# Optimization experiments

Measured on AMD Instinct MI355X. Metric: run time of the kernel, lower is better.

The kernel has to match this reference:

```python
import jax, jax.numpy as jnp
import numpy as np

N_NODES = 50000
N_EDGES = 800000
D_IN = 128
D_OUT = 128
NEG_SLOPE = 0.2


def setup_inputs() -> dict:
    key = jax.random.key(0)
    ks = jax.random.split(key, 6)
    stdv = 1.0 / np.sqrt(D_OUT)
    X = jax.random.normal(ks[0], (N_NODES, D_IN), dtype=jnp.float32)
    W = jax.random.uniform(ks[1], (D_IN, D_OUT), dtype=jnp.float32, minval=-stdv, maxval=stdv)
    W_r = jax.random.uniform(ks[2], (D_IN, D_OUT), dtype=jnp.float32, minval=-stdv, maxval=stdv)
    W_l = jax.random.uniform(ks[3], (D_IN, D_OUT), dtype=jnp.float32, minval=-stdv, maxval=stdv)
    src = jax.random.randint(ks[4], (N_EDGES,), 0, N_NODES, dtype=jnp.int32)
    dst = jax.random.randint(ks[5], (N_EDGES,), 0, N_NODES, dtype=jnp.int32)
    return {"X": X, "W": W, "W_r": W_r, "W_l": W_l, "src": src, "dst": dst}


def reference(X, W, W_r, W_l, src, dst):
    # Dense transforms (comb/agg feature paths)
    comb = X @ W            # [N, D_out]
    h_r = X @ W_r           # [N, D_out]
    h_l = X @ W_l           # [N, D_out]
    # SDDMM: per-edge score e_ij = dot(h_l[i], h_r[j]) at nonzeros of A
    e = jnp.sum(h_l[src] * h_r[dst], axis=-1)          # [E]
    e = jax.nn.leaky_relu(e, negative_slope=NEG_SLOPE)  # LeakyReLU(0.2) on edge values
    # SpMM aggregation: agg[i] = sum_{j in N(i)} e_ij * comb[j]
    msgs = e[:, None] * comb[dst]                       # [E, D_out]
    agg = jax.ops.segment_sum(msgs, src, num_segments=N_NODES)  # [N, D_out]
    return agg
```

## Files before the change

kernel.cpp:

```cpp
#include <hip/hip_runtime.h>
#include <hip/hip_bf16.h>

#define N_NODES 50000
#define N_EDGES 800000
#define D 128
#define NEG_SLOPE 0.2f
#define APAD 136

#define FB 196
#define BCAP 8192
#define CHUNK 2048
#define BIN_NBLK ((N_EDGES + CHUNK - 1) / CHUNK)
#define GROWS 64
#define GGRID ((N_NODES + GROWS - 1) / GROWS)
#define GEMM_LDS (D * APAD * 2 + GROWS * APAD * 2)

typedef __attribute__((ext_vector_type(8))) short bf16x8;
typedef __attribute__((ext_vector_type(4))) float f32x4;

__device__ inline unsigned short f2bf(float f) {
    union { float f; unsigned u; } v; v.f = f;
    const unsigned r = v.u + 0x7FFF + ((v.u >> 16) & 1);
    return (unsigned short)(r >> 16);
}
__device__ inline unsigned fbits(float f) { union { float f; unsigned u; } v; v.f = f; return v.u; }
__device__ inline float ffrom(unsigned u) { union { unsigned u; float f; } v; v.u = u; return v.f; }

__device__ inline void unpack8(const float4 raw, float* o) {
    const unsigned w0 = fbits(raw.x), w1 = fbits(raw.y), w2 = fbits(raw.z), w3 = fbits(raw.w);
    o[0] = ffrom(w0 << 16); o[1] = ffrom(w0 & 0xffff0000u);
    o[2] = ffrom(w1 << 16); o[3] = ffrom(w1 & 0xffff0000u);
    o[4] = ffrom(w2 << 16); o[5] = ffrom(w2 & 0xffff0000u);
    o[6] = ffrom(w3 << 16); o[7] = ffrom(w3 & 0xffff0000u);
}

__device__ inline int scan256_incl(int* arr, int t, int v) {
    arr[t] = v; __syncthreads();
#pragma unroll
    for (int off = 1; off < 256; off <<= 1) {
        const int u = (t >= off) ? arr[t - off] : 0;
        __syncthreads();
        arr[t] += u;
        __syncthreads();
    }
    return arr[t];
}

__device__ __forceinline__ void stage_B_lds(unsigned short* Bs, const ushort* __restrict__ BT) {
    const int tid = threadIdx.x;
#pragma unroll
    for (int i = 0; i < 8; ++i) {
        const int idx = tid + i * 256;
        const int row = idx >> 4;
        const int c8 = (idx & 15) << 3;
        const float4 v = ((const float4*)BT)[idx];
        *(float4*)&Bs[row * APAD + c8] = v;
    }
}

template <bool OUT_F32>
__device__ __forceinline__ void mfma_from_lds(const unsigned short* Bs,
                                              const unsigned short* As,
                                              int rb, float* __restrict__ Cf,
                                              ushort* __restrict__ Cb, int nrows) {
    const int tid = threadIdx.x;
    const int w = tid >> 6, lane = tid & 63, m = lane & 15, kq = lane >> 4;
    f32x4 acc[8] = {};
    const unsigned short* Arow = &As[(w * 16 + m) * APAD + kq * 8];
#pragma unroll
    for (int kc = 0; kc < 4; ++kc) {
        const bf16x8 af = *(const bf16x8*)(Arow + kc * 32);
#pragma unroll
        for (int t2 = 0; t2 < 8; ++t2) {
            const bf16x8 bf = *(const bf16x8*)&Bs[(t2 * 16 + m) * APAD + kc * 32 + kq * 8];
            acc[t2] = __builtin_amdgcn_mfma_f32_16x16x32_bf16(af, bf, acc[t2], 0, 0, 0);
        }
    }
    const int orow0 = rb + w * 16 + kq * 4;
#pragma unroll
    for (int t2 = 0; t2 < 8; ++t2) {
#pragma unroll
        for (int r = 0; r < 4; ++r) {
            const int row = orow0 + r;
            if (row < nrows) {
                const size_t o = (size_t)row * D + t2 * 16 + m;
                if (OUT_F32) Cf[o] = acc[t2][r];
                else         Cb[o] = f2bf(acc[t2][r]);
            }
        }
    }
}

__global__ __launch_bounds__(256) void prep_kernel(const float* __restrict__ W_l,
                                                   const float* __restrict__ W_r,
                                                   const float* __restrict__ W,
                                                   ushort* __restrict__ MbT,
                                                   ushort* __restrict__ WbT,
                                                   int* __restrict__ bucket_fill) {
    if (blockIdx.x == 0) bucket_fill[threadIdx.x] = 0;
    const int a = blockIdx.x * 2 + (threadIdx.x >> 7);
    const int b2 = threadIdx.x & 127;
    float acc = 0.f;
#pragma unroll
    for (int c = 0; c < D; c += 4) {
        const float4 wl = *(const float4*)(W_l + a * D + c);
        const float4 wr = *(const float4*)(W_r + b2 * D + c);
        acc += wl.x * wr.x + wl.y * wr.y + wl.z * wr.z + wl.w * wr.w;
    }
    MbT[b2 * D + a] = f2bf(acc);
    WbT[b2 * D + a] = f2bf(W[a * D + b2]);
}

__global__ __launch_bounds__(256) void k1_kernel(const int* __restrict__ src,
                                                 const int* __restrict__ dst,
                                                 int* __restrict__ bucket_fill,
                                                 int2* __restrict__ binned,
                                                 const ushort* __restrict__ MbT,
                                                 const float4* __restrict__ Xf4,
                                                 ushort* __restrict__ Xb,
                                                 ushort* __restrict__ hMb) {
    __shared__ __align__(16) char smem[GEMM_LDS];
    const int bx = blockIdx.x;
    const int t = threadIdx.x;

    if (bx < BIN_NBLK) {
        int*  hist     = (int*)smem;
        int*  bstart   = hist + 256;
        int*  reserveS = bstart + 256;
        int*  fillL    = reserveS + 256;
        int2* pairs    = (int2*)(fillL + 256);
        int*  targ     = (int*)(pairs + CHUNK);
        const int e0 = bx * CHUNK;

        hist[t] = 0;
        __syncthreads();

        int s[8], d[8], b[8];
#pragma unroll
        for (int i = 0; i < 8; ++i) {
            const int e = e0 + i * 256 + t;
            if (e < N_EDGES) {
                s[i] = src[e]; d[i] = dst[e]; b[i] = s[i] >> 8;
                atomicAdd(&hist[b[i]], 1);
            } else b[i] = -1;
        }
        __syncthreads();
        const int hv = hist[t];
        const int incl = scan256_incl(bstart, t, hv);
        const int mystart = incl - hv;
        reserveS[t] = hv ? atomicAdd(&bucket_fill[t], hv) : 0;
        __syncthreads();
        bstart[t] = mystart;
        fillL[t] = mystart;
        __syncthreads();
#pragma unroll
        for (int i = 0; i < 8; ++i) {
            if (b[i] >= 0) {
                const int p = atomicAdd(&fillL[b[i]], 1);
                pairs[p] = make_int2(s[i], d[i]);
                const int pos = reserveS[b[i]] + (p - bstart[b[i]]);
                targ[p] = (pos < BCAP) ? (b[i] * BCAP + pos) : -1;
            }
        }
        __syncthreads();
        const int nval = min(CHUNK, N_EDGES - e0);
        for (int j = t; j < nval; j += 256)
            if (targ[j] >= 0) binned[targ[j]] = pairs[j];
    } else {
        unsigned short* Bs = (unsigned short*)smem;
        unsigned short* As = Bs + D * APAD;
        const int rb = (bx - BIN_NBLK) * GROWS;

        stage_B_lds(Bs, MbT);
#pragma unroll
        for (int i = 0; i < 4; ++i) {
            const int f2 = t + i * 256;
            const int row = f2 >> 4;
            const int c8 = (f2 & 15) << 3;
            ushort4 lo = {0, 0, 0, 0}, hi = {0, 0, 0, 0};
            if (rb + row < N_NODES) {
                const float4 a = Xf4[(size_t)(rb + row) * 32 + (c8 >> 2)];
                const float4 b = Xf4[(size_t)(rb + row) * 32 + (c8 >> 2) + 1];
                lo.x = f2bf(a.x); lo.y = f2bf(a.y); lo.z = f2bf(a.z); lo.w = f2bf(a.w);
                hi.x = f2bf(b.x); hi.y = f2bf(b.y); hi.z = f2bf(b.z); hi.w = f2bf(b.w);
                ushort* gp = Xb + (size_t)(rb + row) * D + c8;
                *(ushort4*)gp = lo;
                *(ushort4*)(gp + 4) = hi;
            }
            *(ushort4*)&As[row * APAD + c8] = lo;
            *(ushort4*)&As[row * APAD + c8 + 4] = hi;
        }
        __syncthreads();
        mfma_from_lds<false>(Bs, As, rb, nullptr, hMb, N_NODES);
    }
}

__global__ __launch_bounds__(512) void fine_kernel(const int2* __restrict__ binned,
                                                   const int* __restrict__ bucket_fill,
                                                   int* __restrict__ offsets,
                                                   int* __restrict__ sorted_dst) {
    __shared__ int cntS[256];
    __shared__ int nh[256];
    __shared__ int ex[256];
    __shared__ int fill[256];
    __shared__ int dstbuf[BCAP];
    const int b = blockIdx.x;
    const int t = threadIdx.x;

    if (t < 256) cntS[t] = (t < FB) ? bucket_fill[t] : 0;
    __syncthreads();
#pragma unroll
    for (int off = 1; off < 256; off <<= 1) {
        const int u = (t >= off && t < 256) ? cntS[t - off] : 0;
        __syncthreads();
        if (t < 256) cntS[t] += u;
        __syncthreads();
    }
    const int base = (b == 0) ? 0 : cntS[b - 1];
    int cnt = cntS[b] - base;
    if (cnt > BCAP) cnt = BCAP;

    if (t < 256) nh[t] = 0;
    __syncthreads();
    const int2* bb = binned + (size_t)b * BCAP;
    for (int e = t; e < cnt; e += 512) atomicAdd(&nh[bb[e].x & 255], 1);
    __syncthreads();
    const int v = (t < 256) ? nh[t] : 0;
    if (t < 256) ex[t] = v;
    __syncthreads();
#pragma unroll
    for (int off = 1; off < 256; off <<= 1) {
        const int u = (t >= off && t < 256) ? ex[t - off] : 0;
        __syncthreads();
        if (t < 256) ex[t] += u;
        __syncthreads();
    }
    if (t < 256) {
        const int mystart = ex[t] - v;
        const int node = b * 256 + t;
        if (node < N_NODES) offsets[node] = base + mystart;
        fill[t] = mystart;
    }
    __syncthreads();
    for (int e = t; e < cnt; e += 512) {
        const int2 sd = bb[e];
        const int p = atomicAdd(&fill[sd.x & 255], 1);
        dstbuf[p] = sd.y;
    }
    __syncthreads();
    for (int j = t; j < cnt; j += 512)
        sorted_dst[base + j] = dstbuf[j];
}

__global__ __launch_bounds__(256) void spmm_kernel(const ushort* __restrict__ hMb,
                                                   const ushort* __restrict__ Xb,
                                                   const int* __restrict__ offsets,
                                                   const int* __restrict__ sorted_dst,
                                                   ushort* __restrict__ aggXb) {
    const int wave = threadIdx.x >> 6;
    const int lane = threadIdx.x & 63;
    const int node = blockIdx.x * 4 + wave;
    const int q = lane >> 4;
    const int ql = lane & 15;

    float hm[8];
    unpack8(*(const float4*)(hMb + (size_t)node * D + ql * 8), hm);

    const int start = offsets[node];
    const int end = (node == N_NODES - 1) ? N_EDGES : offsets[node + 1];

    float acc[8] = {0.f, 0.f, 0.f, 0.f, 0.f, 0.f, 0.f, 0.f};

    int idx = start + q;
    while (idx + 12 < end) {
        const int d0 = sorted_dst[idx];
        const int d1 = sorted_dst[idx + 4];
        const int d2 = sorted_dst[idx + 8];
        const int d3 = sorted_dst[idx + 12];
        const float4 r0 = *(const float4*)(Xb + (size_t)d0 * D + ql * 8);
        const float4 r1 = *(const float4*)(Xb + (size_t)d1 * D + ql * 8);
        const float4 r2 = *(const float4*)(Xb + (size_t)d2 * D + ql * 8);
        const float4 r3 = *(const float4*)(Xb + (size_t)d3 * D + ql * 8);
        float t0 = 0.f, t1 = 0.f, t2 = 0.f, t3 = 0.f;
        {
            float x[8];
            unpack8(r0, x);
#pragma unroll
            for (int j = 0; j < 8; ++j) t0 = fmaf(hm[j], x[j], t0);
            unpack8(r1, x);
#pragma unroll
            for (int j = 0; j < 8; ++j) t1 = fmaf(hm[j], x[j], t1);
            unpack8(r2, x);
#pragma unroll
            for (int j = 0; j < 8; ++j) t2 = fmaf(hm[j], x[j], t2);
            unpack8(r3, x);
#pragma unroll
            for (int j = 0; j < 8; ++j) t3 = fmaf(hm[j], x[j], t3);
        }
#pragma unroll
        for (int mm = 1; mm < 16; mm <<= 1) {
            t0 += __shfl_xor(t0, mm);
            t1 += __shfl_xor(t1, mm);
            t2 += __shfl_xor(t2, mm);
            t3 += __shfl_xor(t3, mm);
        }
        const float e0 = t0 > 0.f ? t0 : NEG_SLOPE * t0;
        const float e1 = t1 > 0.f ? t1 : NEG_SLOPE * t1;
        const float e2 = t2 > 0.f ? t2 : NEG_SLOPE * t2;
        const float e3 = t3 > 0.f ? t3 : NEG_SLOPE * t3;
        {
            float x[8];
            unpack8(r0, x);
#pragma unroll
            for (int j = 0; j < 8; ++j) acc[j] = fmaf(e0, x[j], acc[j]);
            unpack8(r1, x);
#pragma unroll
            for (int j = 0; j < 8; ++j) acc[j] = fmaf(e1, x[j], acc[j]);
            unpack8(r2, x);
#pragma unroll
            for (int j = 0; j < 8; ++j) acc[j] = fmaf(e2, x[j], acc[j]);
            unpack8(r3, x);
#pragma unroll
            for (int j = 0; j < 8; ++j) acc[j] = fmaf(e3, x[j], acc[j]);
        }
        idx += 16;
    }
    while (idx < end) {
        const int d0 = sorted_dst[idx];
        const float4 r0 = *(const float4*)(Xb + (size_t)d0 * D + ql * 8);
        float x[8];
        unpack8(r0, x);
        float t0 = 0.f;
#pragma unroll
        for (int j = 0; j < 8; ++j) t0 = fmaf(hm[j], x[j], t0);
#pragma unroll
        for (int mm = 1; mm < 16; mm <<= 1) t0 += __shfl_xor(t0, mm);
        const float e0 = t0 > 0.f ? t0 : NEG_SLOPE * t0;
#pragma unroll
        for (int j = 0; j < 8; ++j) acc[j] = fmaf(e0, x[j], acc[j]);
        idx += 4;
    }

#pragma unroll
    for (int j = 0; j < 8; ++j) {
        acc[j] += __shfl_xor(acc[j], 16);
        acc[j] += __shfl_xor(acc[j], 32);
    }
    if (q == 0) {
        ushort4 o0, o1;
        o0.x = f2bf(acc[0]); o0.y = f2bf(acc[1]); o0.z = f2bf(acc[2]); o0.w = f2bf(acc[3]);
        o1.x = f2bf(acc[4]); o1.y = f2bf(acc[5]); o1.z = f2bf(acc[6]); o1.w = f2bf(acc[7]);
        ushort* outp = aggXb + (size_t)node * D + ql * 8;
        *(ushort4*)outp = o0;
        *(ushort4*)(outp + 4) = o1;
    }
}

__global__ __launch_bounds__(256) void gemm2_kernel(const ushort* __restrict__ A,
                                                    const ushort* __restrict__ BT,
                                                    float* __restrict__ Cf) {
    __shared__ __align__(16) char smem[GEMM_LDS];
    unsigned short* Bs = (unsigned short*)smem;
    unsigned short* As = Bs + D * APAD;
    const int tid = threadIdx.x;
    const int rb = blockIdx.x * GROWS;

    stage_B_lds(Bs, BT);
#pragma unroll
    for (int i = 0; i < 4; ++i) {
        const int idx = tid + i * 256;
        const int row = idx >> 4;
        const int c8 = (idx & 15) << 3;
        float4 v = {0.f, 0.f, 0.f, 0.f};
        if (rb + row < N_NODES)
            v = ((const float4*)(A + (size_t)(rb + row) * D))[idx & 15];
        *(float4*)&As[row * APAD + c8] = v;
    }
    __syncthreads();
    mfma_from_lds<true>(Bs, As, rb, Cf, nullptr, N_NODES);
}

extern "C" void kernel_launch(void* const* d_in, const int* in_sizes, int n_in,
                              void* d_out, int out_size, void* d_ws, size_t ws_size,
                              hipStream_t stream) {
    const float* X   = (const float*)d_in[0];
    const float* W   = (const float*)d_in[1];
    const float* W_r = (const float*)d_in[2];
    const float* W_l = (const float*)d_in[3];
    const int* src   = (const int*)d_in[4];
    const int* dst   = (const int*)d_in[5];
    float* agg = (float*)d_out;

    ushort* Xb          = (ushort*)d_ws;
    ushort* hMb         = Xb + (size_t)N_NODES * D;
    ushort* aggXb       = hMb + (size_t)N_NODES * D;
    ushort* MbT         = aggXb + (size_t)N_NODES * D;
    ushort* WbT         = MbT + D * D;
    int*    offsets     = (int*)(WbT + D * D);
    int*    sorted_dst  = offsets + N_NODES;
    int*    bucket_fill = sorted_dst + N_EDGES;
    int2*   binned      = (int2*)(bucket_fill + 256);

    prep_kernel<<<64, 256, 0, stream>>>(W_l, W_r, W, MbT, WbT, bucket_fill);

    k1_kernel<<<BIN_NBLK + GGRID, 256, 0, stream>>>(
        src, dst, bucket_fill, binned, MbT, (const float4*)X, Xb, hMb);

    fine_kernel<<<FB, 512, 0, stream>>>(binned, bucket_fill, offsets, sorted_dst);

    spmm_kernel<<<N_NODES / 4, 256, 0, stream>>>(hMb, Xb, offsets, sorted_dst, aggXb);

    gemm2_kernel<<<GGRID, 256, 0, stream>>>(aggXb, WbT, agg);
}
```

Baseline: 169.6 us.

## Use wave-shuffle block scans and split fine bucket sort across two blocks

Replaces the LDS Hillis-Steele 256-element scans, which need two barriers per step, with wave-level shuffle scans combined through per-wave partial sums, in both the binning and fine-sort kernels. The fine kernel now launches two blocks per bucket, each scattering only the destinations for its half of the 256 nodes. This doubles parallelism on the 196-bucket stage, which otherwise underfills the GPU. The cost is that both halves re-read the whole bucket for the histogram and the scatter, doubling that global traffic.

```diff
diff --git a/kernel.cpp b/kernel.cpp
--- a/kernel.cpp
+++ b/kernel.cpp
@@ -34,16 +34,26 @@
     o[6] = ffrom(w3 << 16); o[7] = ffrom(w3 & 0xffff0000u);
 }
 
-__device__ inline int scan256_incl(int* arr, int t, int v) {
-    arr[t] = v; __syncthreads();
-#pragma unroll
-    for (int off = 1; off < 256; off <<= 1) {
-        const int u = (t >= off) ? arr[t - off] : 0;
-        __syncthreads();
-        arr[t] += u;
-        __syncthreads();
-    }
-    return arr[t];
+__device__ inline int wave_incl_scan(int v, int lane) {
+#pragma unroll
+    for (int off = 1; off < 64; off <<= 1) {
+        const int u = __shfl_up(v, off);
+        if (lane >= off) v += u;
+    }
+    return v;
+}
+
+__device__ inline int block_scan256(int v, int* partial4) {
+    const int t = threadIdx.x, lane = t & 63, w = t >> 6;
+    const int s = wave_incl_scan(v, lane);
+    if (lane == 63) partial4[w] = s;
+    __syncthreads();
+    int add = 0;
+#pragma unroll
+    for (int i = 0; i < 3; ++i)
+        if (i < w) add += partial4[i];
+    __syncthreads();
+    return s + add;
 }
 
 __device__ __forceinline__ void stage_B_lds(unsigned short* Bs, const ushort* __restrict__ BT) {
@@ -128,7 +138,8 @@
         int*  bstart   = hist + 256;
         int*  reserveS = bstart + 256;
         int*  fillL    = reserveS + 256;
-        int2* pairs    = (int2*)(fillL + 256);
+        int*  partial4 = fillL + 256;
+        int2* pairs    = (int2*)(partial4 + 8);
         int*  targ     = (int*)(pairs + CHUNK);
         const int e0 = bx * CHUNK;
 
@@ -146,10 +157,9 @@
         }
         __syncthreads();
         const int hv = hist[t];
-        const int incl = scan256_incl(bstart, t, hv);
+        const int incl = block_scan256(hv, partial4);
         const int mystart = incl - hv;
         reserveS[t] = hv ? atomicAdd(&bucket_fill[t], hv) : 0;
-        __syncthreads();
         bstart[t] = mystart;
         fillL[t] = mystart;
         __syncthreads();
@@ -200,56 +210,76 @@
                                                    int* __restrict__ offsets,
                                                    int* __restrict__ sorted_dst) {
     __shared__ int cntS[256];
+    __shared__ int nstart[256];
     __shared__ int nh[256];
-    __shared__ int ex[256];
     __shared__ int fill[256];
+    __shared__ int partial[8];
     __shared__ int dstbuf[BCAP];
-    const int b = blockIdx.x;
+    const int bx = blockIdx.x;
+    const int bkt = bx >> 1, half = bx & 1;
     const int t = threadIdx.x;
-
-    if (t < 256) cntS[t] = (t < FB) ? bucket_fill[t] : 0;
-    __syncthreads();
-#pragma unroll
-    for (int off = 1; off < 256; off <<= 1) {
-        const int u = (t >= off && t < 256) ? cntS[t - off] : 0;
-        __syncthreads();
-        if (t < 256) cntS[t] += u;
-        __syncthreads();
-    }
-    const int base = (b == 0) ? 0 : cntS[b - 1];
-    int cnt = cntS[b] - base;
+    const int lane = t & 63, w = t >> 6;
+
+    {
+        const int v = (t < FB) ? bucket_fill[t] : 0;
+        const int s = (t < 256) ? wave_incl_scan(v, lane) : 0;
+        if (t < 256 && lane == 63) partial[w] = s;
+        __syncthreads();
+        if (t < 256) {
+            int add = 0;
+#pragma unroll
+            for (int i = 0; i < 3; ++i)
+                if (i < w) add += partial[i];
+            cntS[t] = s + add;
+        }
+        __syncthreads();
+    }
+    const int base = (bkt == 0) ? 0 : cntS[bkt - 1];
+    int cnt = cntS[bkt] - base;
     if (cnt > BCAP) cnt = BCAP;
 
     if (t < 256) nh[t] = 0;
     __syncthreads();
-    const int2* bb = binned + (size_t)b * BCAP;
+    const int2* bb = binned + (size_t)bkt * BCAP;
     for (int e = t; e < cnt; e += 512) atomicAdd(&nh[bb[e].x & 255], 1);
     __syncthreads();
-    const int v = (t < 256) ? nh[t] : 0;
-    if (t < 256) ex[t] = v;
-    __syncthreads();
-#pragma unroll
-    for (int off = 1; off < 256; off <<= 1) {
-        const int u = (t >= off && t < 256) ? ex[t - off] : 0;
-        __syncthreads();
-        if (t < 256) ex[t] += u;
-        __syncthreads();
-    }
-    if (t < 256) {
-        const int mystart = ex[t] - v;
-        const int node = b * 256 + t;
-        if (node < N_NODES) offsets[node] = base + mystart;
-        fill[t] = mystart;
-    }
-    __syncthreads();
+
+    {
+        const int v = (t < 256) ? nh[t] : 0;
+        const int s = (t < 256) ? wave_incl_scan(v, lane) : 0;
+        if (t < 256 && lane == 63) partial[w] = s;
+        __syncthreads();
+        if (t < 256) {
+            int add = 0;
+#pragma unroll
+            for (int i = 0; i < 3; ++i)
+                if (i < w) add += partial[i];
+            nstart[t] = s + add - v;
+            fill[t] = s + add - v;
+        }
+        __syncthreads();
+    }
+
+    if (half == 0 && t < 256) {
+        const int node = bkt * 256 + t;
+        if (node < N_NODES) offsets[node] = base + nstart[t];
+    }
+
+    const int myStart = nstart[half << 7];
+    const int myEnd = half ? cnt : nstart[128];
+
     for (int e = t; e < cnt; e += 512) {
         const int2 sd = bb[e];
-        const int p = atomicAdd(&fill[sd.x & 255], 1);
-        dstbuf[p] = sd.y;
-    }
-    __syncthreads();
-    for (int j = t; j < cnt; j += 512)
-        sorted_dst[base + j] = dstbuf[j];
+        const int nib = sd.x & 255;
+        if ((nib >> 7) == half) {
+            const int p = atomicAdd(&fill[nib], 1);
+            dstbuf[p - myStart] = sd.y;
+        }
+    }
+    __syncthreads();
+    const int mycnt = myEnd - myStart;
+    for (int j = t; j < mycnt; j += 512)
+        sorted_dst[base + myStart + j] = dstbuf[j];
 }
 
 __global__ __launch_bounds__(256) void spmm_kernel(const ushort* __restrict__ hMb,
@@ -406,7 +436,7 @@
     k1_kernel<<<BIN_NBLK + GGRID, 256, 0, stream>>>(
         src, dst, bucket_fill, binned, MbT, (const float4*)X, Xb, hMb);
 
-    fine_kernel<<<FB, 512, 0, stream>>>(binned, bucket_fill, offsets, sorted_dst);
+    fine_kernel<<<FB * 2, 512, 0, stream>>>(binned, bucket_fill, offsets, sorted_dst);
 
     spmm_kernel<<<N_NODES / 4, 256, 0, stream>>>(hMb, Xb, offsets, sorted_dst, aggXb);
 
```

After: 172.3 us. Within noise of the previous version (+1.6%).
